# Kernel optimization log

Hardware: AMD Instinct MI355X
Metric: run time of the kernel (lower is better)

## Reference

```python
import jax, jax.numpy as jnp
import numpy as np

HID = 64


def _lstm_cell(x, h, c, Wih, Whh, bih, bhh):
    # gates: [B, 4*HID], PyTorch LSTMCell gate order: i, f, g, o
    gates = x @ Wih.T + bih + h @ Whh.T + bhh
    i, f, g, o = jnp.split(gates, 4, axis=-1)
    c_new = jax.nn.sigmoid(f) * c + jax.nn.sigmoid(i) * jnp.tanh(g)
    h_new = jax.nn.sigmoid(o) * jnp.tanh(c_new)
    return h_new, c_new


def setup_inputs() -> dict:
    key = jax.random.key(0)
    ks = jax.random.split(key, 11)
    B = 131072
    s_in2 = 1.0 / np.sqrt(2.0)
    s_h = 1.0 / np.sqrt(HID)
    return {
        "train_agent": jax.random.normal(ks[0], (B, 20, 2), jnp.float32),
        "enc_Wih": jax.random.uniform(ks[1], (4 * HID, 2), jnp.float32, -s_h, s_h),
        "enc_Whh": jax.random.uniform(ks[2], (4 * HID, HID), jnp.float32, -s_h, s_h),
        "enc_bih": jax.random.uniform(ks[3], (4 * HID,), jnp.float32, -s_h, s_h),
        "enc_bhh": jax.random.uniform(ks[4], (4 * HID,), jnp.float32, -s_h, s_h),
        "dec_Wih": jax.random.uniform(ks[5], (4 * HID, HID), jnp.float32, -s_h, s_h),
        "dec_Whh": jax.random.uniform(ks[6], (4 * HID, HID), jnp.float32, -s_h, s_h),
        "dec_bih": jax.random.uniform(ks[7], (4 * HID,), jnp.float32, -s_h, s_h),
        "dec_bhh": jax.random.uniform(ks[8], (4 * HID,), jnp.float32, -s_h, s_h),
        "lin_W": jax.random.uniform(ks[9], (2, HID), jnp.float32, -s_h, s_h),
        "lin_b": jax.random.uniform(ks[10], (2,), jnp.float32, -s_h, s_h),
    }


def reference(train_agent, enc_Wih, enc_Whh, enc_bih, enc_bhh,
              dec_Wih, dec_Whh, dec_bih, dec_bhh, lin_W, lin_b):
    B = train_agent.shape[0]
    h0 = jnp.zeros((B, HID), train_agent.dtype)
    c0 = jnp.zeros((B, HID), train_agent.dtype)

    # Encoder: 20 sequential LSTMCell steps over [B, 20, 2]
    def enc_step(carry, x_t):
        h, c = carry
        h, c = _lstm_cell(x_t, h, c, enc_Wih, enc_Whh, enc_bih, enc_bhh)
        return (h, c), None

    xs = jnp.swapaxes(train_agent, 0, 1)  # [20, B, 2]
    (h, c), _ = jax.lax.scan(enc_step, (h0, c0), xs)

    # Decoder: 30 steps, feeding h back in as input; emit Linear(h)
    def dec_step(carry, _):
        h, c = carry
        h, c = _lstm_cell(h, h, c, dec_Wih, dec_Whh, dec_bih, dec_bhh)
        out = h @ lin_W.T + lin_b  # [B, 2]
        return (h, c), out

    (_, _), outs = jax.lax.scan(dec_step, (h, c), None, length=30)
    return jnp.swapaxes(outs, 0, 1)  # [B, 30, 2]
```

## Files before the change

### kernel.cpp

```cpp
#include <hip/hip_runtime.h>


#define LOG2E 1.44269504088896340736f
#define TWO_LOG2E 2.88539008177792681472f

typedef __attribute__((ext_vector_type(4))) short short4v;
typedef __attribute__((ext_vector_type(4))) float float4v;
typedef _Float16 __attribute__((ext_vector_type(8))) half8v;

#if defined(__HIP_DEVICE_COMPILE__)
#define MFMAH(a, b, c) __builtin_amdgcn_mfma_f32_16x16x32_f16((a), (b), (c), 0, 0, 0)
#else
#define MFMAH(a, b, c) (c)
#endif

__device__ __forceinline__ float4v exp2v4(float4v x) {
  float4v r;
  r[0] = __builtin_amdgcn_exp2f(x[0]);
  r[1] = __builtin_amdgcn_exp2f(x[1]);
  r[2] = __builtin_amdgcn_exp2f(x[2]);
  r[3] = __builtin_amdgcn_exp2f(x[3]);
  return r;
}
__device__ __forceinline__ float4v rcpv4(float4v x) {
  float4v r;
  r[0] = __builtin_amdgcn_rcpf(x[0]);
  r[1] = __builtin_amdgcn_rcpf(x[1]);
  r[2] = __builtin_amdgcn_rcpf(x[2]);
  r[3] = __builtin_amdgcn_rcpf(x[3]);
  return r;
}

__device__ __forceinline__ void cellact(const float4v* a, float4v& c,
                                        short4v& hh) {
  const float4v one = {1.f, 1.f, 1.f, 1.f};
  const float4v clo = {-36.f, -36.f, -36.f, -36.f};
  const float4v chi = {36.f, 36.f, 36.f, 36.f};
  float4v Ei = exp2v4(a[0]);
  float4v Ef = exp2v4(a[1]);
  float4v Eg = exp2v4(a[2]);
  float4v Eo = exp2v4(a[3]);
  float4v t1 = one + Ei;
  float4v t2 = one + Eg;
  float4v t3 = one + Ef;
  float4v t4s = Eg * TWO_LOG2E - TWO_LOG2E;
  float4v P = t1 * t2;
  float4v num = c * P + t4s * t3;
  float4v cs = num * rcpv4(P * t3);
  c = cs;
  float4v cl = __builtin_elementwise_min(__builtin_elementwise_max(cs, clo), chi);
  float4v Ec = exp2v4(cl);
  float4v h = (Ec - one) * rcpv4((one + Ec) * (one + Eo));
#pragma unroll
  for (int r = 0; r < 4; ++r) {
    _Float16 hf = (_Float16)h[r];
    hh[r] = (short)__builtin_bit_cast(unsigned short, hf);
  }
}

__global__ __launch_bounds__(256, 3) void lstm_fused(
    const float* __restrict__ x,
    const float* __restrict__ eWih,
    const float* __restrict__ eWhh,
    const float* __restrict__ ebih,
    const float* __restrict__ ebhh,
    const float* __restrict__ dWih,
    const float* __restrict__ dWhh,
    const float* __restrict__ dbih,
    const float* __restrict__ dbhh,
    const float* __restrict__ linW,
    const float* __restrict__ linb,
    float* __restrict__ out,
    int B) {
  const int tid = threadIdx.x;
  const int w   = tid >> 6;
  const int l   = tid & 63;
  const int m   = l & 15;
  const int tg  = l >> 4;
  const int msk = m & 14;
  const int wslot = (((w << 2) | tg) ^ msk) << 2;
  const int bg  = blockIdx.x * 32;

  __shared__ __align__(16) unsigned short Hh[2][32][64];
  __shared__ __align__(16) float Xs[32][42];

  {
    const size_t xoff = (size_t)blockIdx.x * 1280;
    for (int i = tid; i < 1280; i += 256) {
      int mm = i / 40, r = i - mm * 40;
      float v = (xoff + i < (size_t)B * 40) ? x[xoff + i] : 0.0f;
      Xs[mm][r] = v;
    }
  }

  half8v eA[4][2];
  float4v ebs[4], eWa[4], eWb[4];
#pragma unroll
  for (int gi = 0; gi < 4; ++gi) {
    const float gsc = (gi == 2) ? TWO_LOG2E : -LOG2E;
    const int nA = m + 16 * (4 * gi + w);
#pragma unroll
    for (int q = 0; q < 2; ++q) {
      const float* wp = &eWhh[nA * 64 + 32 * q + 8 * tg];
      float4v w0 = *(const float4v*)wp;
      float4v w1 = *(const float4v*)(wp + 4);
      half8v hi;
#pragma unroll
      for (int e = 0; e < 4; ++e) {
        hi[e]     = (_Float16)(w0[e] * gsc);
        hi[4 + e] = (_Float16)(w1[e] * gsc);
      }
      eA[gi][q] = hi;
    }
#pragma unroll
    for (int r = 0; r < 4; ++r) {
      const int n = 64 * gi + 16 * w + 4 * tg + r;
      ebs[gi][r] = (ebih[n] + ebhh[n]) * gsc;
      eWa[gi][r] = eWih[n * 2 + 0] * gsc;
      eWb[gi][r] = eWih[n * 2 + 1] * gsc;
    }
  }

  __syncthreads();

  float4v c0 = {0.f, 0.f, 0.f, 0.f}, c1 = {0.f, 0.f, 0.f, 0.f};
  const half8v z8 = {0, 0, 0, 0, 0, 0, 0, 0};
  half8v b0[2] = {z8, z8}, b1[2] = {z8, z8};
  int p = 0;

#pragma unroll 2
  for (int st = 0; st < 20; ++st) {
    short4v hh0, hh1;
    {
      const float xa0 = Xs[m][2 * st], xb0 = Xs[m][2 * st + 1];
      float4v a0[4];
#pragma unroll
      for (int gi = 0; gi < 4; ++gi) {
        float4v i0 = eWa[gi] * xa0 + (eWb[gi] * xb0 + ebs[gi]);
        float4v a = MFMAH(eA[gi][0], b0[0], i0);
        a0[gi] = MFMAH(eA[gi][1], b0[1], a);
      }
      cellact(a0, c0, hh0);
    }
    {
      const float xa1 = Xs[m + 16][2 * st], xb1 = Xs[m + 16][2 * st + 1];
      float4v a1[4];
#pragma unroll
      for (int gi = 0; gi < 4; ++gi) {
        float4v i1 = eWa[gi] * xa1 + (eWb[gi] * xb1 + ebs[gi]);
        float4v b = MFMAH(eA[gi][0], b1[0], i1);
        a1[gi] = MFMAH(eA[gi][1], b1[1], b);
      }
      cellact(a1, c1, hh1);
    }
    *(short4v*)&Hh[p][m][wslot]      = hh0;
    *(short4v*)&Hh[p][m + 16][wslot] = hh1;
    __syncthreads();
#pragma unroll
    for (int q = 0; q < 2; ++q) {
      const int rs = (((8 * q) | (2 * tg)) ^ msk) << 2;
      b0[q] = *(const half8v*)&Hh[p][m][rs];
      b1[q] = *(const half8v*)&Hh[p][m + 16][rs];
    }
    p ^= 1;
  }

  half8v dA[4][2];
  float4v dbsv[4];
#pragma unroll
  for (int gi = 0; gi < 4; ++gi) {
    const float gsc = (gi == 2) ? TWO_LOG2E : -LOG2E;
    const int nA = m + 16 * (4 * gi + w);
#pragma unroll
    for (int q = 0; q < 2; ++q) {
      const float* wpa = &dWih[nA * 64 + 32 * q + 8 * tg];
      const float* wpb = &dWhh[nA * 64 + 32 * q + 8 * tg];
      float4v a0v = *(const float4v*)wpa;
      float4v a1v = *(const float4v*)(wpa + 4);
      float4v b0v = *(const float4v*)wpb;
      float4v b1v = *(const float4v*)(wpb + 4);
      half8v hi;
#pragma unroll
      for (int e = 0; e < 4; ++e) {
        hi[e]     = (_Float16)((a0v[e] + b0v[e]) * gsc);
        hi[4 + e] = (_Float16)((a1v[e] + b1v[e]) * gsc);
      }
      dA[gi][q] = hi;
    }
#pragma unroll
    for (int r = 0; r < 4; ++r) {
      const int n = 64 * gi + 16 * w + 4 * tg + r;
      dbsv[gi][r] = (dbih[n] + dbhh[n]) * gsc;
    }
  }

  half8v LA[2];
#pragma unroll
  for (int q = 0; q < 2; ++q) {
    half8v hi;
#pragma unroll
    for (int e = 0; e < 4; ++e) {
      const int k0 = 32 * q + 8 * tg + e;
      float v0 = (m < 2) ? linW[m * 64 + k0] : 0.0f;
      float v1 = (m < 2) ? linW[m * 64 + k0 + 4] : 0.0f;
      hi[e] = (_Float16)v0;
      hi[4 + e] = (_Float16)v1;
    }
    LA[q] = hi;
  }
  float4v lbinit = {0.f, 0.f, 0.f, 0.f};
  if (tg == 0) { lbinit[0] = linb[0]; lbinit[1] = linb[1]; }

#pragma unroll 2
  for (int st = 0; st < 30; ++st) {
    short4v hh0, hh1;
    {
      float4v a0[4];
#pragma unroll
      for (int gi = 0; gi < 4; ++gi) {
        float4v a = MFMAH(dA[gi][0], b0[0], dbsv[gi]);
        a0[gi] = MFMAH(dA[gi][1], b0[1], a);
      }
      cellact(a0, c0, hh0);
    }
    {
      float4v a1[4];
#pragma unroll
      for (int gi = 0; gi < 4; ++gi) {
        float4v b = MFMAH(dA[gi][0], b1[0], dbsv[gi]);
        a1[gi] = MFMAH(dA[gi][1], b1[1], b);
      }
      cellact(a1, c1, hh1);
    }
    *(short4v*)&Hh[p][m][wslot]      = hh0;
    *(short4v*)&Hh[p][m + 16][wslot] = hh1;
    __syncthreads();
#pragma unroll
    for (int q = 0; q < 2; ++q) {
      const int rs = (((8 * q) | (2 * tg)) ^ msk) << 2;
      b0[q] = *(const half8v*)&Hh[p][m][rs];
      b1[q] = *(const half8v*)&Hh[p][m + 16][rs];
    }
    if (w == 0) {
      float4v la = lbinit;
      la = MFMAH(LA[0], b0[0], la);
      la = MFMAH(LA[1], b0[1], la);
      if (l < 16 && (bg + l) < B) {
        size_t oidx = ((size_t)(bg + l) * 30 + st) * 2;
        *(float2*)&out[oidx] = make_float2(la[0], la[1]);
      }
    } else if (w == 1) {
      float4v la = lbinit;
      la = MFMAH(LA[0], b1[0], la);
      la = MFMAH(LA[1], b1[1], la);
      if (l < 16 && (bg + 16 + l) < B) {
        size_t oidx = ((size_t)(bg + 16 + l) * 30 + st) * 2;
        *(float2*)&out[oidx] = make_float2(la[0], la[1]);
      }
    }
    p ^= 1;
  }
}

extern "C" void kernel_launch(void* const* d_in, const int* in_sizes, int n_in,
                              void* d_out, int out_size, void* d_ws, size_t ws_size,
                              hipStream_t stream) {
  (void)n_in; (void)out_size; (void)d_ws; (void)ws_size;
  const float* x    = (const float*)d_in[0];
  const float* eWih = (const float*)d_in[1];
  const float* eWhh = (const float*)d_in[2];
  const float* ebih = (const float*)d_in[3];
  const float* ebhh = (const float*)d_in[4];
  const float* dWih = (const float*)d_in[5];
  const float* dWhh = (const float*)d_in[6];
  const float* dbih = (const float*)d_in[7];
  const float* dbhh = (const float*)d_in[8];
  const float* linW = (const float*)d_in[9];
  const float* linb = (const float*)d_in[10];

  const int B = in_sizes[0] / 40;
  const int grid = (B + 31) / 32;
  lstm_fused<<<grid, 256, 0, stream>>>(x, eWih, eWhh, ebih, ebhh,
                                       dWih, dWhh, dbih, dbhh, linW, linb,
                                       (float*)d_out, B);
}
```

Before: 448.3 us.

## Move LSTM weight fragments to LDS and fold input projection into MFMA

Per-thread MFMA weight fragments for the encoder, decoder and output linear layer are now kept in a shared-memory table and reloaded each step instead of held in registers. The encoder's input projection and bias become an extra fp16 MFMA with x packed as half pairs plus a constant 1 lane. Loop unrolling drops to 1. The aim is to cut register pressure for higher occupancy and fewer VALU FMAs, at the cost of extra LDS reads every step, about 40KB more LDS per block, and fp16 rounding of inputs and biases.

```diff
diff --git a/kernel.cpp b/kernel.cpp
--- a/kernel.cpp
+++ b/kernel.cpp
@@ -6,6 +6,7 @@
 
 typedef __attribute__((ext_vector_type(4))) short short4v;
 typedef __attribute__((ext_vector_type(4))) float float4v;
+typedef __attribute__((ext_vector_type(4))) unsigned int uint4v;
 typedef _Float16 __attribute__((ext_vector_type(8))) half8v;
 
 #if defined(__HIP_DEVICE_COMPILE__)
@@ -81,20 +82,27 @@
   const int wslot = (((w << 2) | tg) ^ msk) << 2;
   const int bg  = blockIdx.x * 32;
 
+  __shared__ __align__(16) unsigned short WL[10][256][8];
   __shared__ __align__(16) unsigned short Hh[2][32][64];
-  __shared__ __align__(16) float Xs[32][42];
+  __shared__ unsigned int Xs16[32][21];
+
+  const half8v hz8 = {0, 0, 0, 0, 0, 0, 0, 0};
+  const float4v zf = {0.f, 0.f, 0.f, 0.f};
 
   {
     const size_t xoff = (size_t)blockIdx.x * 1280;
-    for (int i = tid; i < 1280; i += 256) {
-      int mm = i / 40, r = i - mm * 40;
-      float v = (xoff + i < (size_t)B * 40) ? x[xoff + i] : 0.0f;
-      Xs[mm][r] = v;
-    }
-  }
-
-  half8v eA[4][2];
-  float4v ebs[4], eWa[4], eWb[4];
+    for (int i = tid; i < 640; i += 256) {
+      int mm = i / 20, st = i - mm * 20;
+      size_t g = xoff + (size_t)mm * 40 + st * 2;
+      float xa = 0.f, xb = 0.f;
+      if (g + 1 < (size_t)B * 40) { xa = x[g]; xb = x[g + 1]; }
+      unsigned ua = __builtin_bit_cast(unsigned short, (_Float16)xa);
+      unsigned ub = __builtin_bit_cast(unsigned short, (_Float16)xb);
+      Xs16[mm][st] = (ub << 16) | ua;
+    }
+  }
+
+  half8v eA2[4];
 #pragma unroll
   for (int gi = 0; gi < 4; ++gi) {
     const float gsc = (gi == 2) ? TWO_LOG2E : -LOG2E;
@@ -110,46 +118,51 @@
         hi[e]     = (_Float16)(w0[e] * gsc);
         hi[4 + e] = (_Float16)(w1[e] * gsc);
       }
-      eA[gi][q] = hi;
-    }
-#pragma unroll
-    for (int r = 0; r < 4; ++r) {
-      const int n = 64 * gi + 16 * w + 4 * tg + r;
-      ebs[gi][r] = (ebih[n] + ebhh[n]) * gsc;
-      eWa[gi][r] = eWih[n * 2 + 0] * gsc;
-      eWb[gi][r] = eWih[n * 2 + 1] * gsc;
-    }
+      *(half8v*)&WL[gi * 2 + q][tid][0] = hi;
+    }
+    half8v a2 = hz8;
+    if (tg == 0) {
+      a2[0] = (_Float16)(eWih[nA * 2 + 0] * gsc);
+      a2[1] = (_Float16)(eWih[nA * 2 + 1] * gsc);
+      a2[2] = (_Float16)((ebih[nA] + ebhh[nA]) * gsc);
+    }
+    eA2[gi] = a2;
   }
 
   __syncthreads();
 
   float4v c0 = {0.f, 0.f, 0.f, 0.f}, c1 = {0.f, 0.f, 0.f, 0.f};
-  const half8v z8 = {0, 0, 0, 0, 0, 0, 0, 0};
-  half8v b0[2] = {z8, z8}, b1[2] = {z8, z8};
+  half8v b0[2] = {hz8, hz8}, b1[2] = {hz8, hz8};
   int p = 0;
 
-#pragma unroll 2
+#pragma unroll 1
   for (int st = 0; st < 20; ++st) {
     short4v hh0, hh1;
     {
-      const float xa0 = Xs[m][2 * st], xb0 = Xs[m][2 * st + 1];
+      uint4v t; t[0] = Xs16[m][st]; t[1] = 0x3C00u; t[2] = 0u; t[3] = 0u;
+      half8v bq2 = (tg == 0) ? __builtin_bit_cast(half8v, t) : hz8;
       float4v a0[4];
 #pragma unroll
       for (int gi = 0; gi < 4; ++gi) {
-        float4v i0 = eWa[gi] * xa0 + (eWb[gi] * xb0 + ebs[gi]);
-        float4v a = MFMAH(eA[gi][0], b0[0], i0);
-        a0[gi] = MFMAH(eA[gi][1], b0[1], a);
+        half8v f0 = *(const half8v*)&WL[gi * 2 + 0][tid][0];
+        half8v f1 = *(const half8v*)&WL[gi * 2 + 1][tid][0];
+        float4v a = MFMAH(eA2[gi], bq2, zf);
+        a = MFMAH(f0, b0[0], a);
+        a0[gi] = MFMAH(f1, b0[1], a);
       }
       cellact(a0, c0, hh0);
     }
     {
-      const float xa1 = Xs[m + 16][2 * st], xb1 = Xs[m + 16][2 * st + 1];
+      uint4v t; t[0] = Xs16[m + 16][st]; t[1] = 0x3C00u; t[2] = 0u; t[3] = 0u;
+      half8v bq2 = (tg == 0) ? __builtin_bit_cast(half8v, t) : hz8;
       float4v a1[4];
 #pragma unroll
       for (int gi = 0; gi < 4; ++gi) {
-        float4v i1 = eWa[gi] * xa1 + (eWb[gi] * xb1 + ebs[gi]);
-        float4v b = MFMAH(eA[gi][0], b1[0], i1);
-        a1[gi] = MFMAH(eA[gi][1], b1[1], b);
+        half8v f0 = *(const half8v*)&WL[gi * 2 + 0][tid][0];
+        half8v f1 = *(const half8v*)&WL[gi * 2 + 1][tid][0];
+        float4v a = MFMAH(eA2[gi], bq2, zf);
+        a = MFMAH(f0, b1[0], a);
+        a1[gi] = MFMAH(f1, b1[1], a);
       }
       cellact(a1, c1, hh1);
     }
@@ -165,7 +178,6 @@
     p ^= 1;
   }
 
-  half8v dA[4][2];
   float4v dbsv[4];
 #pragma unroll
   for (int gi = 0; gi < 4; ++gi) {
@@ -185,7 +197,7 @@
         hi[e]     = (_Float16)((a0v[e] + b0v[e]) * gsc);
         hi[4 + e] = (_Float16)((a1v[e] + b1v[e]) * gsc);
       }
-      dA[gi][q] = hi;
+      *(half8v*)&WL[gi * 2 + q][tid][0] = hi;
     }
 #pragma unroll
     for (int r = 0; r < 4; ++r) {
@@ -193,33 +205,34 @@
       dbsv[gi][r] = (dbih[n] + dbhh[n]) * gsc;
     }
   }
-
-  half8v LA[2];
 #pragma unroll
   for (int q = 0; q < 2; ++q) {
-    half8v hi;
-#pragma unroll
-    for (int e = 0; e < 4; ++e) {
-      const int k0 = 32 * q + 8 * tg + e;
-      float v0 = (m < 2) ? linW[m * 64 + k0] : 0.0f;
-      float v1 = (m < 2) ? linW[m * 64 + k0 + 4] : 0.0f;
-      hi[e] = (_Float16)v0;
-      hi[4 + e] = (_Float16)v1;
-    }
-    LA[q] = hi;
+    half8v hi = hz8;
+    if (m < 2) {
+      const int k0 = 32 * q + 8 * tg;
+#pragma unroll
+      for (int e = 0; e < 4; ++e) {
+        hi[e]     = (_Float16)linW[m * 64 + k0 + e];
+        hi[4 + e] = (_Float16)linW[m * 64 + k0 + e + 4];
+      }
+    }
+    *(half8v*)&WL[8 + q][tid][0] = hi;
   }
   float4v lbinit = {0.f, 0.f, 0.f, 0.f};
   if (tg == 0) { lbinit[0] = linb[0]; lbinit[1] = linb[1]; }
-
-#pragma unroll 2
+  __syncthreads();
+
+#pragma unroll 1
   for (int st = 0; st < 30; ++st) {
     short4v hh0, hh1;
     {
       float4v a0[4];
 #pragma unroll
       for (int gi = 0; gi < 4; ++gi) {
-        float4v a = MFMAH(dA[gi][0], b0[0], dbsv[gi]);
-        a0[gi] = MFMAH(dA[gi][1], b0[1], a);
+        half8v f0 = *(const half8v*)&WL[gi * 2 + 0][tid][0];
+        half8v f1 = *(const half8v*)&WL[gi * 2 + 1][tid][0];
+        float4v a = MFMAH(f0, b0[0], dbsv[gi]);
+        a0[gi] = MFMAH(f1, b0[1], a);
       }
       cellact(a0, c0, hh0);
     }
@@ -227,8 +240,10 @@
       float4v a1[4];
 #pragma unroll
       for (int gi = 0; gi < 4; ++gi) {
-        float4v b = MFMAH(dA[gi][0], b1[0], dbsv[gi]);
-        a1[gi] = MFMAH(dA[gi][1], b1[1], b);
+        half8v f0 = *(const half8v*)&WL[gi * 2 + 0][tid][0];
+        half8v f1 = *(const half8v*)&WL[gi * 2 + 1][tid][0];
+        float4v a = MFMAH(f0, b1[0], dbsv[gi]);
+        a1[gi] = MFMAH(f1, b1[1], a);
       }
       cellact(a1, c1, hh1);
     }
@@ -242,17 +257,21 @@
       b1[q] = *(const half8v*)&Hh[p][m + 16][rs];
     }
     if (w == 0) {
+      half8v L0 = *(const half8v*)&WL[8][tid][0];
+      half8v L1 = *(const half8v*)&WL[9][tid][0];
       float4v la = lbinit;
-      la = MFMAH(LA[0], b0[0], la);
-      la = MFMAH(LA[1], b0[1], la);
+      la = MFMAH(L0, b0[0], la);
+      la = MFMAH(L1, b0[1], la);
       if (l < 16 && (bg + l) < B) {
         size_t oidx = ((size_t)(bg + l) * 30 + st) * 2;
         *(float2*)&out[oidx] = make_float2(la[0], la[1]);
       }
     } else if (w == 1) {
+      half8v L0 = *(const half8v*)&WL[8][tid][0];
+      half8v L1 = *(const half8v*)&WL[9][tid][0];
       float4v la = lbinit;
-      la = MFMAH(LA[0], b1[0], la);
-      la = MFMAH(LA[1], b1[1], la);
+      la = MFMAH(L0, b1[0], la);
+      la = MFMAH(L1, b1[1], la);
       if (l < 16 && (bg + 16 + l) < B) {
         size_t oidx = ((size_t)(bg + 16 + l) * 30 + st) * 2;
         *(float2*)&out[oidx] = make_float2(la[0], la[1]);
```

Result: faster. 432.6 us (median of 2 runs) (-3.5%).
